# Kernel tuning notes

Hardware: AMD Instinct MI355X
Metric: run time of the kernel (lower is better)

## Reference

```python
import jax, jax.numpy as jnp
import numpy as np

H = 56; W = 56; WS = 7; SS = 3; HEADS = 12; DIM = 384

def _rel_pos_index(ws):
    coords = np.stack(np.meshgrid(np.arange(ws), np.arange(ws), indexing='ij'))  # (2, ws, ws)
    cf = coords.reshape(2, -1)
    rel = (cf[:, :, None] - cf[:, None, :]).transpose(1, 2, 0).astype(np.int64)  # (N, N, 2)
    rel[:, :, 0] += ws - 1
    rel[:, :, 1] += ws - 1
    rel[:, :, 0] *= 2 * ws - 1
    return jnp.asarray(rel.sum(-1))  # (N, N)

def _attn_mask(h, w, ws, ss):
    img = np.zeros((h, w))
    cnt = 0
    for hs in (slice(0, -ws), slice(-ws, -ss), slice(-ss, None)):
        for wsl in (slice(0, -ws), slice(-ws, -ss), slice(-ss, None)):
            img[hs, wsl] = cnt
            cnt += 1
    mw = img.reshape(h // ws, ws, w // ws, ws).transpose(0, 2, 1, 3).reshape(-1, ws * ws)
    am = mw[:, None, :] - mw[:, :, None]
    return jnp.asarray(np.where(am != 0, -100.0, 0.0).astype(np.float32))  # (nW, N, N)

REL_IDX = _rel_pos_index(WS)
ATTN_MASK = _attn_mask(H, W, WS, SS)

def _ln(x, g, b):
    mu = x.mean(-1, keepdims=True)
    var = x.var(-1, keepdims=True)  # biased, matches torch LayerNorm
    return (x - mu) / jnp.sqrt(var + 1e-5) * g + b

def setup_inputs():
    key = jax.random.key(0)
    ks = jax.random.split(key, 8)
    C = DIM
    Hd = 4 * C
    s = lambda k, shp: jax.random.normal(k, shp, jnp.float32) * 0.02
    return dict(
        x=jax.random.normal(ks[0], (32, H * W, C), jnp.float32),
        norm1_g=jnp.ones((C,), jnp.float32), norm1_b=jnp.zeros((C,), jnp.float32),
        qkv_w=s(ks[1], (3 * C, C)), qkv_b=jnp.zeros((3 * C,), jnp.float32),
        rpb_table=s(ks[2], ((2 * WS - 1) ** 2, HEADS)),
        proj_w=s(ks[3], (C, C)), proj_b=jnp.zeros((C,), jnp.float32),
        norm2_g=jnp.ones((C,), jnp.float32), norm2_b=jnp.zeros((C,), jnp.float32),
        fc1_w=s(ks[4], (Hd, C)), fc1_b=jnp.zeros((Hd,), jnp.float32),
        fc2_w=s(ks[5], (C, Hd)), fc2_b=jnp.zeros((C,), jnp.float32),
    )

def reference(x, norm1_g, norm1_b, qkv_w, qkv_b, rpb_table, proj_w, proj_b,
              norm2_g, norm2_b, fc1_w, fc1_b, fc2_w, fc2_b):
    B, L, C = x.shape
    h = HEADS
    d = C // h
    N = WS * WS
    nW = (H // WS) * (W // WS)
    shortcut = x
    y = _ln(x, norm1_g, norm1_b).reshape(B, H, W, C)
    # cyclic shift
    y = jnp.roll(y, (-SS, -SS), axis=(1, 2))
    # window partition -> (B*nW, N, C)
    y = y.reshape(B, H // WS, WS, W // WS, WS, C).transpose(0, 1, 3, 2, 4, 5).reshape(B * nW, N, C)
    # windowed attention
    qkv = (y @ qkv_w.T + qkv_b).reshape(B * nW, N, 3, h, d).transpose(2, 0, 3, 1, 4)
    q, k, v = qkv[0], qkv[1], qkv[2]  # (B*nW, h, N, d)
    scale = d ** -0.5
    attn = jnp.einsum('whnd,whmd->whnm', q * scale, k)
    bias = rpb_table[REL_IDX.reshape(-1)].reshape(N, N, h).transpose(2, 0, 1)  # (h, N, N)
    attn = attn + bias[None]
    attn = attn.reshape(B, nW, h, N, N) + ATTN_MASK[None, :, None]
    attn = jax.nn.softmax(attn.reshape(B * nW, h, N, N), axis=-1)
    out = jnp.einsum('whnm,whmd->whnd', attn, v).transpose(0, 2, 1, 3).reshape(B * nW, N, C)
    out = out @ proj_w.T + proj_b
    # window reverse -> (B, H, W, C)
    out = out.reshape(B, H // WS, W // WS, WS, WS, C).transpose(0, 1, 3, 2, 4, 5).reshape(B, H, W, C)
    # reverse cyclic shift
    out = jnp.roll(out, (SS, SS), axis=(1, 2)).reshape(B, L, C)
    x = shortcut + out
    m = _ln(x, norm2_g, norm2_b)
    m = jax.nn.gelu(m @ fc1_w.T + fc1_b, approximate=False) @ fc2_w.T + fc2_b
    return x + m
```

## Files before the change

kernel.cpp:

```cpp
#include <hip/hip_runtime.h>
#include <cstdint>
#include <cstddef>

typedef __bf16 bf16;
typedef __bf16 bf16x8 __attribute__((ext_vector_type(8)));
typedef float f32x4 __attribute__((ext_vector_type(4)));

__global__ __launch_bounds__(256) void k_cvtw(
    const float* __restrict__ w0, const float* __restrict__ w1,
    const float* __restrict__ w2, const float* __restrict__ w3,
    bf16* __restrict__ o)
{
    int i = blockIdx.x * 256 + threadIdx.x;
    float v;
    if (i < 442368)       v = w0[i];
    else if (i < 589824)  v = w1[i - 442368];
    else if (i < 1179648) v = w2[i - 589824];
    else                  v = w3[i - 1179648];
    o[i] = (bf16)v;
}

__device__ __forceinline__ void ln_stats(const float* __restrict__ xp, int lane,
                                         float v[6], float& mean, float& rstd)
{
    float s = 0.f, ss = 0.f;
    #pragma unroll
    for (int j = 0; j < 6; ++j) {
        v[j] = xp[j * 64 + lane];
        s += v[j]; ss += v[j] * v[j];
    }
    #pragma unroll
    for (int o = 32; o; o >>= 1) { s += __shfl_xor(s, o); ss += __shfl_xor(ss, o); }
    mean = s * (1.f / 384.f);
    float var = ss * (1.f / 384.f) - mean * mean;
    rstd = rsqrtf(var + 1e-5f);
}

__global__ __launch_bounds__(256) void k_ln1(
    const float* __restrict__ x, const float* __restrict__ g,
    const float* __restrict__ b, bf16* __restrict__ ywin)
{
    int wv = threadIdx.x >> 6, lane = threadIdx.x & 63;
    int tok = blockIdx.x * 4 + wv;
    float v[6], mean, rstd;
    ln_stats(x + (size_t)tok * 384, lane, v, mean, rstd);
    int bi = tok / 3136, l = tok - bi * 3136;
    int h = l / 56, w = l - h * 56;
    int hs = h + 53; if (hs >= 56) hs -= 56;
    int ws = w + 53; if (ws >= 56) ws -= 56;
    int m = (bi * 64 + (hs / 7) * 8 + (ws / 7)) * 49 + (hs % 7) * 7 + (ws % 7);
    bf16* op = ywin + (size_t)m * 384;
    #pragma unroll
    for (int j = 0; j < 6; ++j) {
        int ch = j * 64 + lane;
        op[ch] = (bf16)((v[j] - mean) * rstd * g[ch] + b[ch]);
    }
}

__global__ __launch_bounds__(256) void k_ln2(
    const float* __restrict__ x, const float* __restrict__ g,
    const float* __restrict__ b, bf16* __restrict__ y)
{
    int wv = threadIdx.x >> 6, lane = threadIdx.x & 63;
    int tok = blockIdx.x * 4 + wv;
    float v[6], mean, rstd;
    ln_stats(x + (size_t)tok * 384, lane, v, mean, rstd);
    bf16* op = y + (size_t)tok * 384;
    #pragma unroll
    for (int j = 0; j < 6; ++j) {
        int ch = j * 64 + lane;
        op[ch] = (bf16)((v[j] - mean) * rstd * g[ch] + b[ch]);
    }
}

template<int EPI>
__global__ __launch_bounds__(256) void k_gemm(
    const bf16* __restrict__ A, const bf16* __restrict__ Bt,
    const float* __restrict__ bias, const float* __restrict__ resid,
    void* __restrict__ out, int N, int K, int nbn)
{
    __shared__ bf16 As[128 * 32];
    __shared__ bf16 Bs[128 * 32];

    int nwg = gridDim.x;
    int bid = blockIdx.x;
    int swz = (bid & 7) * (nwg >> 3) + (bid >> 3);
    int bm = swz / nbn, bn = swz % nbn;

    int tid  = threadIdx.x;
    int lane = tid & 63;
    int wv   = tid >> 6;
    int wr = wv >> 1, wc = wv & 1;
    int lr = lane & 15, lg = lane >> 4;

    int r1 = tid >> 2;
    int sl = (tid & 3) ^ ((tid >> 3) & 3);
    int la1 = r1 * 32 + sl * 8;
    int la2 = la1 + 64 * 32;
    const bf16* a1 = A  + (size_t)(bm * 128 + r1) * K + (tid & 3) * 8;
    const bf16* b1 = Bt + (size_t)(bn * 128 + r1) * K + (tid & 3) * 8;
    const bf16* a2 = a1 + (size_t)64 * K;
    const bf16* b2 = b1 + (size_t)64 * K;

    f32x4 acc[4][4] = {};

    uint4 va1 = *(const uint4*)(a1);
    uint4 va2 = *(const uint4*)(a2);
    uint4 vb1 = *(const uint4*)(b1);
    uint4 vb2 = *(const uint4*)(b2);

    for (int k0 = 0; k0 < K; k0 += 32) {
        __syncthreads();
        *(uint4*)&As[la1] = va1;  *(uint4*)&As[la2] = va2;
        *(uint4*)&Bs[la1] = vb1;  *(uint4*)&Bs[la2] = vb2;
        __syncthreads();
        if (k0 + 32 < K) {
            va1 = *(const uint4*)(a1 + k0 + 32);
            va2 = *(const uint4*)(a2 + k0 + 32);
            vb1 = *(const uint4*)(b1 + k0 + 32);
            vb2 = *(const uint4*)(b2 + k0 + 32);
        }
        bf16x8 af[4], bfr[4];
        #pragma unroll
        for (int i = 0; i < 4; ++i) {
            int ra = wr * 64 + i * 16 + lr;
            af[i]  = *(const bf16x8*)&As[ra * 32 + ((lg ^ ((ra >> 1) & 3)) << 3)];
            int rb = wc * 64 + i * 16 + lr;
            bfr[i] = *(const bf16x8*)&Bs[rb * 32 + ((lg ^ ((rb >> 1) & 3)) << 3)];
        }
        #pragma unroll
        for (int mi = 0; mi < 4; ++mi)
            #pragma unroll
            for (int ni = 0; ni < 4; ++ni)
                acc[mi][ni] = __builtin_amdgcn_mfma_f32_16x16x32_bf16(
                    af[mi], bfr[ni], acc[mi][ni], 0, 0, 0);
    }

    int row0 = bm * 128 + wr * 64;
    int col0 = bn * 128 + wc * 64;
    #pragma unroll
    for (int mi = 0; mi < 4; ++mi)
    #pragma unroll
    for (int ni = 0; ni < 4; ++ni)
    #pragma unroll
    for (int r = 0; r < 4; ++r) {
        int gr = row0 + mi * 16 + lg * 4 + r;
        int gc = col0 + ni * 16 + lr;
        float v = acc[mi][ni][r] + bias[gc];
        if constexpr (EPI == 0) {
            if (gc < 384) v *= 0.17677669529663687f;
            ((bf16*)out)[(size_t)gr * N + gc] = (bf16)v;
        } else if constexpr (EPI == 1) {
            int bi = gr / 3136, rem = gr - bi * 3136;
            int win = rem / 49, pos = rem - win * 49;
            int hs = (win >> 3) * 7 + pos / 7;
            int ws = (win & 7) * 7 + pos % 7;
            hs += 3; if (hs >= 56) hs -= 56;
            ws += 3; if (ws >= 56) ws -= 56;
            size_t oi = ((size_t)bi * 3136 + hs * 56 + ws) * 384 + gc;
            ((float*)out)[oi] = resid[oi] + v;
        } else if constexpr (EPI == 2) {
            float ge = 0.5f * v * (1.f + erff(v * 0.70710678118654752f));
            ((bf16*)out)[(size_t)gr * N + gc] = (bf16)ge;
        } else {
            size_t oi = (size_t)gr * 384 + gc;
            ((float*)out)[oi] += v;
        }
    }
}

__global__ __launch_bounds__(64) void k_attn(
    const bf16* __restrict__ qkv, const float* __restrict__ rpb,
    bf16* __restrict__ outb)
{
    __shared__ float k_s[49 * 32];
    __shared__ float v_s[49 * 32];
    __shared__ float s_l[49 * 51];
    __shared__ float bias_s[169];
    __shared__ int   lab_s[49];

    int head   = blockIdx.x % 12;
    int window = blockIdx.x / 12;
    int lane   = threadIdx.x;
    size_t base = (size_t)window * 49 * 1152 + head * 32;

    for (int c = lane; c < 196; c += 64) {
        int pos = c >> 2, d0 = (c & 3) << 3;
        bf16x8 kv = *(const bf16x8*)(qkv + base + 384 + (size_t)pos * 1152 + d0);
        bf16x8 vv = *(const bf16x8*)(qkv + base + 768 + (size_t)pos * 1152 + d0);
        #pragma unroll
        for (int t = 0; t < 8; ++t) {
            k_s[pos * 32 + d0 + t] = (float)kv[t];
            v_s[pos * 32 + d0 + t] = (float)vv[t];
        }
    }
    for (int idx = lane; idx < 169; idx += 64) bias_s[idx] = rpb[idx * 12 + head];
    {
        int win = window & 63;
        int wh = win >> 3, ww = win & 7;
        if (lane < 49) {
            int hs = wh * 7 + lane / 7, ws = ww * 7 + lane % 7;
            int rr = hs < 49 ? 0 : (hs < 53 ? 1 : 2);
            int cc = ws < 49 ? 0 : (ws < 53 ? 1 : 2);
            lab_s[lane] = rr * 3 + cc;
        }
    }
    __syncthreads();
    if (lane >= 49) return;

    int row = lane;
    float qr[32];
    {
        const bf16* qp = qkv + base + (size_t)row * 1152;
        #pragma unroll
        for (int d0 = 0; d0 < 32; d0 += 8) {
            bf16x8 qv = *(const bf16x8*)(qp + d0);
            #pragma unroll
            for (int t = 0; t < 8; ++t) qr[d0 + t] = (float)qv[t];
        }
    }
    int r0 = row / 7, c0 = row - r0 * 7;
    int lab0 = lab_s[row];
    float* srow = &s_l[row * 51];

    float mx = -1e30f;
    for (int j = 0; j < 49; ++j) {
        const float* kp = &k_s[j * 32];
        float d0 = 0.f, d1 = 0.f, d2 = 0.f, d3 = 0.f;
        #pragma unroll
        for (int d = 0; d < 32; d += 4) {
            d0 += qr[d] * kp[d];     d1 += qr[d + 1] * kp[d + 1];
            d2 += qr[d + 2] * kp[d + 2]; d3 += qr[d + 3] * kp[d + 3];
        }
        float dot = (d0 + d1) + (d2 + d3);
        int jr = j / 7, jc = j - jr * 7;
        dot += bias_s[(r0 - jr + 6) * 13 + (c0 - jc + 6)];
        if (lab0 != lab_s[j]) dot -= 100.f;
        srow[j] = dot;
        mx = fmaxf(mx, dot);
    }
    float sum = 0.f;
    for (int j = 0; j < 49; ++j) {
        float e = __expf(srow[j] - mx);
        srow[j] = e; sum += e;
    }
    float rs = 1.f / sum;

    float o[32];
    #pragma unroll
    for (int d = 0; d < 32; ++d) o[d] = 0.f;
    for (int j = 0; j < 49; ++j) {
        float p = srow[j];
        const float* vp = &v_s[j * 32];
        #pragma unroll
        for (int d = 0; d < 32; ++d) o[d] += p * vp[d];
    }
    bf16* op = outb + (size_t)(window * 49 + row) * 384 + head * 32;
    #pragma unroll
    for (int d0 = 0; d0 < 32; d0 += 8) {
        bf16x8 ov;
        #pragma unroll
        for (int t = 0; t < 8; ++t) ov[t] = (bf16)(o[d0 + t] * rs);
        *(bf16x8*)(op + d0) = ov;
    }
}

extern "C" void kernel_launch(void* const* d_in, const int* in_sizes, int n_in,
                              void* d_out, int out_size, void* d_ws, size_t ws_size,
                              hipStream_t stream)
{
    const float* x     = (const float*)d_in[0];
    const float* n1g   = (const float*)d_in[1];
    const float* n1b   = (const float*)d_in[2];
    const float* qkvw  = (const float*)d_in[3];
    const float* qkvb  = (const float*)d_in[4];
    const float* rpb   = (const float*)d_in[5];
    const float* projw = (const float*)d_in[6];
    const float* projb = (const float*)d_in[7];
    const float* n2g   = (const float*)d_in[8];
    const float* n2b   = (const float*)d_in[9];
    const float* fc1w  = (const float*)d_in[10];
    const float* fc1b  = (const float*)d_in[11];
    const float* fc2w  = (const float*)d_in[12];
    const float* fc2b  = (const float*)d_in[13];
    float* out = (float*)d_out;

    char* ws = (char*)d_ws;
    bf16* Wq   = (bf16*)(ws);
    bf16* Wp   = (bf16*)(ws + 884736);
    bf16* W1   = (bf16*)(ws + 1179648);
    bf16* W2   = (bf16*)(ws + 2359296);
    bf16* ywin = (bf16*)(ws + 3538944);
    bf16* qkv  = (bf16*)(ws + 80609280);
    bf16* attn = (bf16*)(ws + 311820288);
    bf16* hbuf = (bf16*)(ws + 80609280);
    bf16* y2   = ywin;

    k_cvtw<<<6912, 256, 0, stream>>>(qkvw, projw, fc1w, fc2w, Wq);
    k_ln1<<<25088, 256, 0, stream>>>(x, n1g, n1b, ywin);
    k_gemm<0><<<784 * 9, 256, 0, stream>>>(ywin, Wq, qkvb, nullptr, qkv, 1152, 384, 9);
    k_attn<<<24576, 64, 0, stream>>>(qkv, rpb, attn);
    k_gemm<1><<<784 * 3, 256, 0, stream>>>(attn, Wp, projb, x, out, 384, 384, 3);
    k_ln2<<<25088, 256, 0, stream>>>(out, n2g, n2b, y2);
    k_gemm<2><<<784 * 12, 256, 0, stream>>>(y2, W1, fc1b, nullptr, hbuf, 1536, 384, 12);
    k_gemm<3><<<784 * 3, 256, 0, stream>>>(hbuf, W2, fc2b, nullptr, out, 384, 1536, 3);
}
```

Measured before the change: 1.384 ms.

## Rewrite window attention on MFMA with fused bias/mask table and direct-to-LDS GEMM loads

Windowed attention is rewritten so each wave handles one head's window with bf16 MFMA for both QK^T and PV. The softmax runs in registers using exp2, with log2e folded into the q scale. A new small kernel precomputes a combined relative-position-bias and shift-mask table per window type and head, padded to 64x64, so the attention kernel does no per-element index or mask logic. The GEMM now loads tiles with global_load_lds instead of staging through registers, and the LayerNorm kernels use float2 loads and packed bf16 stores. The GEMM change drops the previous register prefetch overlap and adds an extra barrier per k-step. The bias table reuses workspace that holds the QKV weights once that GEMM has finished.

Result: faster. 1.229 ms (-11.2%).

```diff
diff --git a/kernel.cpp b/kernel.cpp
--- a/kernel.cpp
+++ b/kernel.cpp
@@ -5,6 +5,19 @@
 typedef __bf16 bf16;
 typedef __bf16 bf16x8 __attribute__((ext_vector_type(8)));
 typedef float f32x4 __attribute__((ext_vector_type(4)));
+typedef unsigned int u32;
+
+__device__ __forceinline__ u32 pk(float a, float b) {
+    u32 ua = __builtin_bit_cast(unsigned short, (bf16)a);
+    u32 ub = __builtin_bit_cast(unsigned short, (bf16)b);
+    return (ub << 16) | ua;
+}
+
+__device__ __forceinline__ void gld16(void* l, const void* g) {
+    __builtin_amdgcn_global_load_lds(
+        (const __attribute__((address_space(1))) void*)(size_t)g,
+        (__attribute__((address_space(3))) void*)l, 16, 0, 0);
+}
 
 __global__ __launch_bounds__(256) void k_cvtw(
     const float* __restrict__ w0, const float* __restrict__ w1,
@@ -20,20 +33,26 @@
     o[i] = (bf16)v;
 }
 
-__device__ __forceinline__ void ln_stats(const float* __restrict__ xp, int lane,
-                                         float v[6], float& mean, float& rstd)
-{
-    float s = 0.f, ss = 0.f;
-    #pragma unroll
-    for (int j = 0; j < 6; ++j) {
-        v[j] = xp[j * 64 + lane];
-        s += v[j]; ss += v[j] * v[j];
-    }
-    #pragma unroll
-    for (int o = 32; o; o >>= 1) { s += __shfl_xor(s, o); ss += __shfl_xor(ss, o); }
-    mean = s * (1.f / 384.f);
-    float var = ss * (1.f / 384.f) - mean * mean;
-    rstd = rsqrtf(var + 1e-5f);
+__global__ __launch_bounds__(256) void k_bias(
+    const float* __restrict__ rpb, float* __restrict__ ft)
+{
+    int t = blockIdx.x;
+    int type = t / 12, head = t - (t / 12) * 12;
+    for (int e = threadIdx.x; e < 4096; e += 256) {
+        int i = e >> 6, j = e & 63;
+        float v;
+        if (j >= 49) v = -1e30f;
+        else if (i >= 49) v = 0.f;
+        else {
+            int ri = i / 7, ci = i - ri * 7, rj = j / 7, cj = j - rj * 7;
+            v = rpb[((ri - rj + 6) * 13 + (ci - cj + 6)) * 12 + head] * 1.4426950408889634f;
+            int li = 0, lj = 0;
+            if (type & 2) { li += (ri < 4) ? 3 : 6; lj += (rj < 4) ? 3 : 6; }
+            if (type & 1) { li += (ci < 4) ? 1 : 2; lj += (cj < 4) ? 1 : 2; }
+            if (li != lj) v -= 144.26950408889634f;
+        }
+        ft[(size_t)t * 4096 + e] = v;
+    }
 }
 
 __global__ __launch_bounds__(256) void k_ln1(
@@ -42,18 +61,32 @@
 {
     int wv = threadIdx.x >> 6, lane = threadIdx.x & 63;
     int tok = blockIdx.x * 4 + wv;
-    float v[6], mean, rstd;
-    ln_stats(x + (size_t)tok * 384, lane, v, mean, rstd);
+    const float2* xp = (const float2*)(x + (size_t)tok * 384);
+    float2 v[3];
+    float s = 0.f, ss = 0.f;
+    #pragma unroll
+    for (int j = 0; j < 3; ++j) {
+        v[j] = xp[j * 64 + lane];
+        s += v[j].x + v[j].y; ss += v[j].x * v[j].x + v[j].y * v[j].y;
+    }
+    #pragma unroll
+    for (int o = 32; o; o >>= 1) { s += __shfl_xor(s, o); ss += __shfl_xor(ss, o); }
+    float mean = s * (1.f / 384.f);
+    float rstd = rsqrtf(ss * (1.f / 384.f) - mean * mean + 1e-5f);
     int bi = tok / 3136, l = tok - bi * 3136;
     int h = l / 56, w = l - h * 56;
     int hs = h + 53; if (hs >= 56) hs -= 56;
     int ws = w + 53; if (ws >= 56) ws -= 56;
     int m = (bi * 64 + (hs / 7) * 8 + (ws / 7)) * 49 + (hs % 7) * 7 + (ws % 7);
-    bf16* op = ywin + (size_t)m * 384;
-    #pragma unroll
-    for (int j = 0; j < 6; ++j) {
-        int ch = j * 64 + lane;
-        op[ch] = (bf16)((v[j] - mean) * rstd * g[ch] + b[ch]);
+    u32* op = (u32*)(ywin + (size_t)m * 384);
+    const float2* g2 = (const float2*)g;
+    const float2* b2 = (const float2*)b;
+    #pragma unroll
+    for (int j = 0; j < 3; ++j) {
+        int c2 = j * 64 + lane;
+        float2 gg = g2[c2], bb = b2[c2];
+        op[c2] = pk((v[j].x - mean) * rstd * gg.x + bb.x,
+                    (v[j].y - mean) * rstd * gg.y + bb.y);
     }
 }
 
@@ -63,13 +96,27 @@
 {
     int wv = threadIdx.x >> 6, lane = threadIdx.x & 63;
     int tok = blockIdx.x * 4 + wv;
-    float v[6], mean, rstd;
-    ln_stats(x + (size_t)tok * 384, lane, v, mean, rstd);
-    bf16* op = y + (size_t)tok * 384;
-    #pragma unroll
-    for (int j = 0; j < 6; ++j) {
-        int ch = j * 64 + lane;
-        op[ch] = (bf16)((v[j] - mean) * rstd * g[ch] + b[ch]);
+    const float2* xp = (const float2*)(x + (size_t)tok * 384);
+    float2 v[3];
+    float s = 0.f, ss = 0.f;
+    #pragma unroll
+    for (int j = 0; j < 3; ++j) {
+        v[j] = xp[j * 64 + lane];
+        s += v[j].x + v[j].y; ss += v[j].x * v[j].x + v[j].y * v[j].y;
+    }
+    #pragma unroll
+    for (int o = 32; o; o >>= 1) { s += __shfl_xor(s, o); ss += __shfl_xor(ss, o); }
+    float mean = s * (1.f / 384.f);
+    float rstd = rsqrtf(ss * (1.f / 384.f) - mean * mean + 1e-5f);
+    u32* op = (u32*)(y + (size_t)tok * 384);
+    const float2* g2 = (const float2*)g;
+    const float2* b2 = (const float2*)b;
+    #pragma unroll
+    for (int j = 0; j < 3; ++j) {
+        int c2 = j * 64 + lane;
+        float2 gg = g2[c2], bb = b2[c2];
+        op[c2] = pk((v[j].x - mean) * rstd * gg.x + bb.x,
+                    (v[j].y - mean) * rstd * gg.y + bb.y);
     }
 }
 
@@ -93,33 +140,23 @@
     int wr = wv >> 1, wc = wv & 1;
     int lr = lane & 15, lg = lane >> 4;
 
-    int r1 = tid >> 2;
-    int sl = (tid & 3) ^ ((tid >> 3) & 3);
-    int la1 = r1 * 32 + sl * 8;
-    int la2 = la1 + 64 * 32;
-    const bf16* a1 = A  + (size_t)(bm * 128 + r1) * K + (tid & 3) * 8;
-    const bf16* b1 = Bt + (size_t)(bn * 128 + r1) * K + (tid & 3) * 8;
-    const bf16* a2 = a1 + (size_t)64 * K;
-    const bf16* b2 = b1 + (size_t)64 * K;
+    int rowL = wv * 32 + (lane >> 2);
+    int seg  = (lane & 3) ^ ((rowL >> 1) & 3);
+    const bf16* ga0 = A  + (size_t)(bm * 128 + rowL) * K + seg * 8;
+    const bf16* gb0 = Bt + (size_t)(bn * 128 + rowL) * K + seg * 8;
+    const bf16* ga1 = ga0 + (size_t)16 * K;
+    const bf16* gb1 = gb0 + (size_t)16 * K;
+    bf16* lA0 = &As[(wv * 32) * 32];
+    bf16* lA1 = &As[(wv * 32 + 16) * 32];
+    bf16* lB0 = &Bs[(wv * 32) * 32];
+    bf16* lB1 = &Bs[(wv * 32 + 16) * 32];
 
     f32x4 acc[4][4] = {};
 
-    uint4 va1 = *(const uint4*)(a1);
-    uint4 va2 = *(const uint4*)(a2);
-    uint4 vb1 = *(const uint4*)(b1);
-    uint4 vb2 = *(const uint4*)(b2);
-
     for (int k0 = 0; k0 < K; k0 += 32) {
+        gld16(lA0, ga0 + k0); gld16(lA1, ga1 + k0);
+        gld16(lB0, gb0 + k0); gld16(lB1, gb1 + k0);
         __syncthreads();
-        *(uint4*)&As[la1] = va1;  *(uint4*)&As[la2] = va2;
-        *(uint4*)&Bs[la1] = vb1;  *(uint4*)&Bs[la2] = vb2;
-        __syncthreads();
-        if (k0 + 32 < K) {
-            va1 = *(const uint4*)(a1 + k0 + 32);
-            va2 = *(const uint4*)(a2 + k0 + 32);
-            vb1 = *(const uint4*)(b1 + k0 + 32);
-            vb2 = *(const uint4*)(b2 + k0 + 32);
-        }
         bf16x8 af[4], bfr[4];
         #pragma unroll
         for (int i = 0; i < 4; ++i) {
@@ -134,6 +171,7 @@
             for (int ni = 0; ni < 4; ++ni)
                 acc[mi][ni] = __builtin_amdgcn_mfma_f32_16x16x32_bf16(
                     af[mi], bfr[ni], acc[mi][ni], 0, 0, 0);
+        __syncthreads();
     }
 
     int row0 = bm * 128 + wr * 64;
@@ -148,7 +186,7 @@
         int gc = col0 + ni * 16 + lr;
         float v = acc[mi][ni][r] + bias[gc];
         if constexpr (EPI == 0) {
-            if (gc < 384) v *= 0.17677669529663687f;
+            if (gc < 384) v *= 0.25498226244716875f;
             ((bf16*)out)[(size_t)gr * N + gc] = (bf16)v;
         } else if constexpr (EPI == 1) {
             int bi = gr / 3136, rem = gr - bi * 3136;
@@ -169,100 +207,152 @@
     }
 }
 
-__global__ __launch_bounds__(64) void k_attn(
-    const bf16* __restrict__ qkv, const float* __restrict__ rpb,
+__global__ __launch_bounds__(256, 3) void k_attn(
+    const bf16* __restrict__ qkv, const float* __restrict__ fusedT,
     bf16* __restrict__ outb)
 {
-    __shared__ float k_s[49 * 32];
-    __shared__ float v_s[49 * 32];
-    __shared__ float s_l[49 * 51];
-    __shared__ float bias_s[169];
-    __shared__ int   lab_s[49];
-
-    int head   = blockIdx.x % 12;
-    int window = blockIdx.x / 12;
-    int lane   = threadIdx.x;
+    __shared__ bf16 vt[4][32 * 64];
+    __shared__ bf16 pl[4][64 * 64];
+
+    int bid = blockIdx.x;
+    int swz = (bid & 7) * (6144 >> 3) + (bid >> 3);
+    int window = swz / 3;
+    int wv = threadIdx.x >> 6, lane = threadIdx.x & 63;
+    int head = (swz - window * 3) * 4 + wv;
+    int lr = lane & 15, lg = lane >> 4;
+
     size_t base = (size_t)window * 49 * 1152 + head * 32;
-
-    for (int c = lane; c < 196; c += 64) {
-        int pos = c >> 2, d0 = (c & 3) << 3;
-        bf16x8 kv = *(const bf16x8*)(qkv + base + 384 + (size_t)pos * 1152 + d0);
-        bf16x8 vv = *(const bf16x8*)(qkv + base + 768 + (size_t)pos * 1152 + d0);
-        #pragma unroll
-        for (int t = 0; t < 8; ++t) {
-            k_s[pos * 32 + d0 + t] = (float)kv[t];
-            v_s[pos * 32 + d0 + t] = (float)vv[t];
-        }
-    }
-    for (int idx = lane; idx < 169; idx += 64) bias_s[idx] = rpb[idx * 12 + head];
-    {
-        int win = window & 63;
-        int wh = win >> 3, ww = win & 7;
-        if (lane < 49) {
-            int hs = wh * 7 + lane / 7, ws = ww * 7 + lane % 7;
-            int rr = hs < 49 ? 0 : (hs < 53 ? 1 : 2);
-            int cc = ws < 49 ? 0 : (ws < 53 ? 1 : 2);
-            lab_s[lane] = rr * 3 + cc;
-        }
-    }
-    __syncthreads();
-    if (lane >= 49) return;
-
-    int row = lane;
-    float qr[32];
-    {
-        const bf16* qp = qkv + base + (size_t)row * 1152;
-        #pragma unroll
-        for (int d0 = 0; d0 < 32; d0 += 8) {
-            bf16x8 qv = *(const bf16x8*)(qp + d0);
-            #pragma unroll
-            for (int t = 0; t < 8; ++t) qr[d0 + t] = (float)qv[t];
-        }
-    }
-    int r0 = row / 7, c0 = row - r0 * 7;
-    int lab0 = lab_s[row];
-    float* srow = &s_l[row * 51];
-
-    float mx = -1e30f;
-    for (int j = 0; j < 49; ++j) {
-        const float* kp = &k_s[j * 32];
-        float d0 = 0.f, d1 = 0.f, d2 = 0.f, d3 = 0.f;
-        #pragma unroll
-        for (int d = 0; d < 32; d += 4) {
-            d0 += qr[d] * kp[d];     d1 += qr[d + 1] * kp[d + 1];
-            d2 += qr[d + 2] * kp[d + 2]; d3 += qr[d + 3] * kp[d + 3];
-        }
-        float dot = (d0 + d1) + (d2 + d3);
-        int jr = j / 7, jc = j - jr * 7;
-        dot += bias_s[(r0 - jr + 6) * 13 + (c0 - jc + 6)];
-        if (lab0 != lab_s[j]) dot -= 100.f;
-        srow[j] = dot;
-        mx = fmaxf(mx, dot);
-    }
-    float sum = 0.f;
-    for (int j = 0; j < 49; ++j) {
-        float e = __expf(srow[j] - mx);
-        srow[j] = e; sum += e;
-    }
-    float rs = 1.f / sum;
-
-    float o[32];
-    #pragma unroll
-    for (int d = 0; d < 32; ++d) o[d] = 0.f;
-    for (int j = 0; j < 49; ++j) {
-        float p = srow[j];
-        const float* vp = &v_s[j * 32];
-        #pragma unroll
-        for (int d = 0; d < 32; ++d) o[d] += p * vp[d];
-    }
-    bf16* op = outb + (size_t)(window * 49 + row) * 384 + head * 32;
-    #pragma unroll
-    for (int d0 = 0; d0 < 32; d0 += 8) {
-        bf16x8 ov;
-        #pragma unroll
-        for (int t = 0; t < 8; ++t) ov[t] = (bf16)(o[d0 + t] * rs);
-        *(bf16x8*)(op + d0) = ov;
-    }
+    const bf16* Qp = qkv + base;
+    const bf16* Kp = qkv + base + 384;
+    const bf16* Vp = qkv + base + 768;
+
+    bf16* vts = vt[wv];
+    #pragma unroll
+    for (int t0 = 0; t0 < 8; ++t0) {
+        int t = t0 * 64 + lane;
+        int d = t >> 4, pos = 48 + (t & 15);
+        vts[d * 64 + ((((pos >> 3) ^ (d & 7)) << 3) | (pos & 7))] = (bf16)0.f;
+    }
+    #pragma unroll
+    for (int t0 = 0; t0 < 4; ++t0) {
+        int t = t0 * 64 + lane;
+        if (t < 196) {
+            int pos = t >> 2, c8 = (t & 3) << 3;
+            bf16x8 vv = *(const bf16x8*)(Vp + (size_t)pos * 1152 + c8);
+            #pragma unroll
+            for (int u = 0; u < 8; ++u) {
+                int d = c8 + u;
+                vts[d * 64 + ((((pos >> 3) ^ (d & 7)) << 3) | (pos & 7))] = vv[u];
+            }
+        }
+    }
+
+    bf16x8 kf[4], qf[4];
+    #pragma unroll
+    for (int t = 0; t < 4; ++t) {
+        int row = t * 16 + lr; row = row > 48 ? 48 : row;
+        kf[t] = *(const bf16x8*)(Kp + (size_t)row * 1152 + lg * 8);
+        qf[t] = *(const bf16x8*)(Qp + (size_t)row * 1152 + lg * 8);
+    }
+    f32x4 st[4][4];
+    #pragma unroll
+    for (int a = 0; a < 4; ++a)
+        #pragma unroll
+        for (int c = 0; c < 4; ++c) st[a][c] = f32x4{0.f, 0.f, 0.f, 0.f};
+    #pragma unroll
+    for (int mj = 0; mj < 4; ++mj)
+        #pragma unroll
+        for (int ni = 0; ni < 4; ++ni)
+            st[mj][ni] = __builtin_amdgcn_mfma_f32_16x16x32_bf16(
+                kf[mj], qf[ni], st[mj][ni], 0, 0, 0);
+
+    int wtype = (((window & 63) >= 56) ? 2 : 0) | (((window & 7) == 7) ? 1 : 0);
+    const float* bt = fusedT + ((size_t)(wtype * 12 + head) << 12);
+    #pragma unroll
+    for (int ni = 0; ni < 4; ++ni)
+        #pragma unroll
+        for (int mj = 0; mj < 4; ++mj) {
+            f32x4 bv = *(const f32x4*)(bt + (ni * 16 + lr) * 64 + mj * 16 + lg * 4);
+            st[mj][ni] += bv;
+        }
+
+    #pragma unroll
+    for (int ni = 0; ni < 4; ++ni) {
+        float mx = -1e30f;
+        #pragma unroll
+        for (int mj = 0; mj < 4; ++mj)
+            mx = fmaxf(mx, fmaxf(fmaxf(st[mj][ni][0], st[mj][ni][1]),
+                                 fmaxf(st[mj][ni][2], st[mj][ni][3])));
+        mx = fmaxf(mx, __shfl_xor(mx, 16));
+        mx = fmaxf(mx, __shfl_xor(mx, 32));
+        float l = 0.f;
+        #pragma unroll
+        for (int mj = 0; mj < 4; ++mj)
+            #pragma unroll
+            for (int r = 0; r < 4; ++r) {
+                float p = exp2f(st[mj][ni][r] - mx);
+                st[mj][ni][r] = p; l += p;
+            }
+        l += __shfl_xor(l, 16);
+        l += __shfl_xor(l, 32);
+        float rl = 1.f / l;
+        #pragma unroll
+        for (int mj = 0; mj < 4; ++mj)
+            #pragma unroll
+            for (int r = 0; r < 4; ++r) st[mj][ni][r] *= rl;
+    }
+
+    bf16* plw = pl[wv];
+    #pragma unroll
+    for (int mj = 0; mj < 4; ++mj)
+        #pragma unroll
+        for (int ni = 0; ni < 4; ++ni)
+            #pragma unroll
+            for (int hh = 0; hh < 2; ++hh) {
+                u32 w = pk(st[mj][ni][hh * 2], st[mj][ni][hh * 2 + 1]);
+                int j = mj * 16 + lg * 4 + hh * 2;
+                int i = ni * 16 + lr;
+                *(u32*)&plw[i * 64 + (((j >> 3) ^ (lr & 7)) << 3) + (j & 7)] = w;
+            }
+
+    bf16x8 pa[4][2], vf[2][2];
+    #pragma unroll
+    for (int mi = 0; mi < 4; ++mi)
+        #pragma unroll
+        for (int kk = 0; kk < 2; ++kk)
+            pa[mi][kk] = *(const bf16x8*)&plw[(mi * 16 + lr) * 64 +
+                                              (((kk * 4 + lg) ^ (lr & 7)) << 3)];
+    #pragma unroll
+    for (int td = 0; td < 2; ++td)
+        #pragma unroll
+        for (int kk = 0; kk < 2; ++kk)
+            vf[td][kk] = *(const bf16x8*)&vts[(td * 16 + lr) * 64 +
+                                              (((kk * 4 + lg) ^ (lr & 7)) << 3)];
+
+    f32x4 o[4][2];
+    #pragma unroll
+    for (int a = 0; a < 4; ++a) { o[a][0] = f32x4{0.f,0.f,0.f,0.f}; o[a][1] = f32x4{0.f,0.f,0.f,0.f}; }
+    #pragma unroll
+    for (int kk = 0; kk < 2; ++kk)
+        #pragma unroll
+        for (int mi = 0; mi < 4; ++mi)
+            #pragma unroll
+            for (int td = 0; td < 2; ++td)
+                o[mi][td] = __builtin_amdgcn_mfma_f32_16x16x32_bf16(
+                    pa[mi][kk], vf[td][kk], o[mi][td], 0, 0, 0);
+
+    bf16* op = outb + (size_t)window * 49 * 384 + head * 32;
+    #pragma unroll
+    for (int mi = 0; mi < 4; ++mi)
+        #pragma unroll
+        for (int r = 0; r < 4; ++r) {
+            int i = mi * 16 + lg * 4 + r;
+            if (i < 49) {
+                #pragma unroll
+                for (int td = 0; td < 2; ++td)
+                    op[(size_t)i * 384 + td * 16 + lr] = (bf16)o[mi][td][r];
+            }
+        }
 }
 
 extern "C" void kernel_launch(void* const* d_in, const int* in_sizes, int n_in,
@@ -295,11 +385,13 @@
     bf16* attn = (bf16*)(ws + 311820288);
     bf16* hbuf = (bf16*)(ws + 80609280);
     bf16* y2   = ywin;
+    float* fusedT = (float*)ws;
 
     k_cvtw<<<6912, 256, 0, stream>>>(qkvw, projw, fc1w, fc2w, Wq);
     k_ln1<<<25088, 256, 0, stream>>>(x, n1g, n1b, ywin);
     k_gemm<0><<<784 * 9, 256, 0, stream>>>(ywin, Wq, qkvb, nullptr, qkv, 1152, 384, 9);
-    k_attn<<<24576, 64, 0, stream>>>(qkv, rpb, attn);
+    k_bias<<<48, 256, 0, stream>>>(rpb, fusedT);
+    k_attn<<<6144, 256, 0, stream>>>(qkv, fusedT, attn);
     k_gemm<1><<<784 * 3, 256, 0, stream>>>(attn, Wp, projb, x, out, 384, 384, 3);
     k_ln2<<<25088, 256, 0, stream>>>(out, n2g, n2b, y2);
     k_gemm<2><<<784 * 12, 256, 0, stream>>>(y2, W1, fc1b, nullptr, hbuf, 1536, 384, 12);
```
